# Kernel optimization log

Measured on AMD Instinct MI355X. Metric: run time of the kernel, lower is better.

## Reference

```python
import jax, jax.numpy as jnp
import numpy as np

NUM_PT = 13
NUM_SQ = 64
SQPT = NUM_SQ * NUM_PT            # 832
NUM_FEATURES = NUM_SQ * SQPT      # 53248
ATTN_TABLE = NUM_SQ * SQPT * SQPT # 44302336
DEPTH = 256
DFF = 1024
NUM_HEADS = 4
N = 512
LN_EPS = 1e-5


def layer_norm(x, w, b):
    m = jnp.mean(x, axis=-1, keepdims=True)
    v = jnp.mean(jnp.square(x - m), axis=-1, keepdims=True)
    return (x - m) * jax.lax.rsqrt(v + LN_EPS) * w + b


def setup_inputs() -> dict:
    key = jax.random.key(0)
    ks = jax.random.split(key, 12)
    # indices must satisfy piece_indices = ksq*832 + offset, offset in [0,832)
    pno = jax.random.randint(ks[0], (N, NUM_SQ), 0, SQPT, dtype=jnp.int32)
    ksq = jax.random.randint(ks[1], (N,), 0, NUM_SQ, dtype=jnp.int32)
    piece_indices = ksq[:, None] * SQPT + pno
    attn_bias_indices = jax.random.randint(ks[2], (N, NUM_SQ * NUM_SQ), 0, NUM_PT * NUM_PT, dtype=jnp.int32)
    f32 = jnp.float32
    return {
        "piece_indices": piece_indices,
        "attn_bias_indices": attn_bias_indices,
        "ksq": ksq,
        "value_table": jax.random.normal(ks[3], (NUM_FEATURES, DEPTH), f32) * 0.02,
        "attn_weights_table": jax.random.normal(ks[4], (ATTN_TABLE, NUM_HEADS), f32) * 0.02,
        "attn_bias_table": jax.random.normal(ks[5], (NUM_PT * NUM_PT, NUM_HEADS), f32) * 0.02,
        "attn_scale": jnp.asarray(100.0, f32),
        "W1": jax.random.normal(ks[6], (DEPTH, DFF), f32) * 0.02,
        "b1": jnp.zeros((DFF,), f32),
        "W2": jax.random.normal(ks[7], (DFF, DEPTH), f32) * 0.02,
        "b2": jnp.zeros((DEPTH,), f32),
        "ln1_w": jnp.ones((DEPTH,), f32),
        "ln1_b": jnp.zeros((DEPTH,), f32),
        "ln2_w": jnp.ones((DEPTH,), f32),
        "ln2_b": jnp.zeros((DEPTH,), f32),
    }


def reference(piece_indices, attn_bias_indices, ksq, value_table, attn_weights_table,
              attn_bias_table, attn_scale, W1, b1, W2, b2, ln1_w, ln1_b, ln2_w, ln2_b):
    n = piece_indices.shape[0]
    dh = DEPTH // NUM_HEADS
    pno = piece_indices - ksq[:, None] * SQPT                      # [N,64] in [0,832)
    attn_idx = (pno[:, :, None] * SQPT + pno[:, None, :]
                + ksq[:, None, None] * SQPT * SQPT)                # [N,64,64]
    aw = attn_weights_table[attn_idx]                              # [N,64,64,H]
    abi = attn_bias_indices.reshape(n, NUM_SQ, NUM_SQ).transpose(0, 2, 1)
    ab = attn_bias_table[abi]                                      # [N,64,64,H]
    logits = ((aw + ab) * attn_scale).transpose(0, 3, 1, 2)        # [N,H,64,64]
    attn = jax.nn.softmax(logits, axis=-1)
    values = value_table[piece_indices].reshape(n, NUM_SQ, NUM_HEADS, dh).transpose(0, 2, 1, 3)  # [N,H,64,dh]
    ctx = jnp.einsum('nhqk,nhkd->nhqd', attn, values) + values
    x = layer_norm(ctx.transpose(0, 2, 1, 3).reshape(n, NUM_SQ, DEPTH), ln1_w, ln1_b)
    ffn = jnp.maximum(x @ W1 + b1, 0.0) @ W2 + b2
    return layer_norm(ffn + x, ln2_w, ln2_b)
```

## Files before the change

### kernel.cpp

```cpp
#include <hip/hip_runtime.h>
#include <stdint.h>

typedef unsigned short u16;
typedef __attribute__((ext_vector_type(8))) short bf16x8;
typedef __attribute__((ext_vector_type(4))) float f32x4;

typedef __attribute__((address_space(1))) const unsigned char gas_u8;
typedef __attribute__((address_space(3))) unsigned char las_u8;

__device__ __forceinline__ void gload_lds16(const void* g, void* l) {
  __builtin_amdgcn_global_load_lds((const gas_u8*)g, (las_u8*)l, 16, 0, 0);
}

__device__ __forceinline__ u16 f2bf(float f) {
  uint32_t u = __float_as_uint(f);
  u += 0x7fffu + ((u >> 16) & 1u);
  return (u16)(u >> 16);
}
__device__ __forceinline__ float bf2f(u16 v) {
  return __uint_as_float(((uint32_t)v) << 16);
}

__global__ __launch_bounds__(256, 4)
void transpose_kernel(const float* __restrict__ W1, u16* __restrict__ W1T,
                      const float* __restrict__ W2, u16* __restrict__ W2T) {
  __shared__ u16 tile[64 * 66];
  int b = blockIdx.x;
  const float* src; u16* dst; int R, C, tc, tr;
  if (b < 64) { src = W1; dst = W1T; R = 256; C = 1024; tc = (b & 15) * 64; tr = (b >> 4) * 64; }
  else { b -= 64; src = W2; dst = W2T; R = 1024; C = 256; tc = (b & 3) * 64; tr = (b >> 2) * 64; }
  const int t = threadIdx.x;
  const int c = t & 63, rb = t >> 6;
#pragma unroll
  for (int i = 0; i < 16; ++i) {
    int r = i * 4 + rb;
    tile[r * 66 + c] = f2bf(src[(size_t)(tr + r) * C + tc + c]);
  }
  __syncthreads();
#pragma unroll
  for (int i = 0; i < 16; ++i) {
    int x = i * 4 + rb;
    int y = c;
    dst[(size_t)(tc + x) * R + tr + y] = tile[y * 66 + x];
  }
}

__global__ __launch_bounds__(256, 2)
void attn_kernel(const int* __restrict__ piece_indices,
                 const int* __restrict__ abi_idx,
                 const int* __restrict__ ksq,
                 const float* __restrict__ value_table,
                 const float* __restrict__ aw_table,
                 const float* __restrict__ ab_table,
                 const float* __restrict__ scale_p,
                 const float* __restrict__ ln1w, const float* __restrict__ ln1b,
                 u16* __restrict__ xout) {
  __shared__ __align__(16) u16 VT[256 * 64];
  __shared__ __align__(16) u16 P[4 * 64 * 64];
  __shared__ __align__(16) float abt_s[169 * 4];
  __shared__ int pno_s[64];
  __shared__ int pidx_s[64];
  __shared__ float red[4][64][2];
  __shared__ float redA[4][4][64];
  __shared__ float redB[4][4][64];

  const int n = blockIdx.x;
  const int t = threadIdx.x;
  const int h = t >> 6;
  const int lane = t & 63;
  const int ks = ksq[n];

  if (t < 64) {
    int pi = piece_indices[n * 64 + t];
    pidx_s[t] = pi;
    pno_s[t] = pi - ks * 832;
  }
  for (int i = t; i < 676; i += 256) abt_s[i] = ab_table[i];
  __syncthreads();

  const float scale = scale_p[0];
  const int q = lane, kg = h;

  float l[4][16];
  {
    const int base = ks * (832 * 832) + pno_s[q] * 832;
#pragma unroll
    for (int j = 0; j < 16; ++j) {
      int k = kg * 16 + j;
      int idx = base + pno_s[k];
      f32x4 aw4 = *(const f32x4*)(aw_table + (size_t)idx * 4);
      int bi = abi_idx[n * 4096 + k * 64 + q];
      f32x4 ab4 = *(const f32x4*)(abt_s + bi * 4);
#pragma unroll
      for (int hh = 0; hh < 4; ++hh) l[hh][j] = (aw4[hh] + ab4[hh]) * scale;
    }
  }

  {
    const int feat = t;
#pragma unroll
    for (int c = 0; c < 8; ++c) {
      bf16x8 vv;
#pragma unroll
      for (int j = 0; j < 8; ++j) {
        int k = c * 8 + j;
        float v = value_table[(size_t)pidx_s[k] * 256 + feat];
        vv[j] = (short)f2bf(v);
      }
      int off = feat * 64 + ((c ^ (feat & 7)) << 3);
      *(bf16x8*)(&VT[off]) = vv;
    }
  }

#pragma unroll
  for (int hh = 0; hh < 4; ++hh) {
    float m = l[hh][0];
#pragma unroll
    for (int j = 1; j < 16; ++j) m = fmaxf(m, l[hh][j]);
    redA[kg][hh][q] = m;
  }
  __syncthreads();
  float gmax[4], inv[4];
#pragma unroll
  for (int hh = 0; hh < 4; ++hh) {
    float m = fmaxf(fmaxf(redA[0][hh][q], redA[1][hh][q]),
                    fmaxf(redA[2][hh][q], redA[3][hh][q]));
    gmax[hh] = m;
    float s = 0.f;
#pragma unroll
    for (int j = 0; j < 16; ++j) { l[hh][j] = __expf(l[hh][j] - m); s += l[hh][j]; }
    redB[kg][hh][q] = s;
  }
  __syncthreads();
#pragma unroll
  for (int hh = 0; hh < 4; ++hh)
    inv[hh] = 1.f / (redB[0][hh][q] + redB[1][hh][q] + redB[2][hh][q] + redB[3][hh][q]);

#pragma unroll
  for (int hh = 0; hh < 4; ++hh) {
#pragma unroll
    for (int c2 = 0; c2 < 2; ++c2) {
      int c = kg * 2 + c2;
      bf16x8 pv;
#pragma unroll
      for (int j8 = 0; j8 < 8; ++j8) {
        int j = c2 * 8 + j8;
        int k = kg * 16 + j;
        float v = l[hh][j] * inv[hh] + ((k == q) ? 1.f : 0.f);
        pv[j8] = (short)f2bf(v);
      }
      int off = (hh * 64 + q) * 64 + ((c ^ (q & 7)) << 3);
      *(bf16x8*)(&P[off]) = pv;
    }
  }
  __syncthreads();

  const int li = lane & 15, lg = lane >> 4;
  f32x4 acc[4][4] = {};
#pragma unroll
  for (int kst = 0; kst < 2; ++kst) {
    int cg = kst * 4 + lg;
    bf16x8 aF[4], bF[4];
#pragma unroll
    for (int mi = 0; mi < 4; ++mi) {
      int row = mi * 16 + li;
      aF[mi] = *(const bf16x8*)(&P[(h * 64 + row) * 64 + ((cg ^ (row & 7)) << 3)]);
    }
#pragma unroll
    for (int ni = 0; ni < 4; ++ni) {
      int rr = h * 64 + ni * 16 + li;
      bF[ni] = *(const bf16x8*)(&VT[rr * 64 + ((cg ^ (rr & 7)) << 3)]);
    }
#pragma unroll
    for (int mi = 0; mi < 4; ++mi)
#pragma unroll
      for (int ni = 0; ni < 4; ++ni)
        acc[mi][ni] = __builtin_amdgcn_mfma_f32_16x16x32_bf16(aF[mi], bF[ni], acc[mi][ni], 0, 0, 0);
  }

#pragma unroll
  for (int mi = 0; mi < 4; ++mi)
#pragma unroll
    for (int r = 0; r < 4; ++r) {
      float s1 = 0.f, s2 = 0.f;
#pragma unroll
      for (int ni = 0; ni < 4; ++ni) { float v = acc[mi][ni][r]; s1 += v; s2 += v * v; }
#pragma unroll
      for (int mk = 1; mk < 16; mk <<= 1) { s1 += __shfl_xor(s1, mk, 64); s2 += __shfl_xor(s2, mk, 64); }
      if (li == 0) { int q2 = mi * 16 + lg * 4 + r; red[h][q2][0] = s1; red[h][q2][1] = s2; }
    }
  __syncthreads();

  float w_[4], b_[4];
#pragma unroll
  for (int ni = 0; ni < 4; ++ni) {
    int f = h * 64 + ni * 16 + li;
    w_[ni] = ln1w[f]; b_[ni] = ln1b[f];
  }
#pragma unroll
  for (int mi = 0; mi < 4; ++mi)
#pragma unroll
    for (int r = 0; r < 4; ++r) {
      int q2 = mi * 16 + lg * 4 + r;
      float S1 = red[0][q2][0] + red[1][q2][0] + red[2][q2][0] + red[3][q2][0];
      float S2 = red[0][q2][1] + red[1][q2][1] + red[2][q2][1] + red[3][q2][1];
      float mean = S1 * (1.f / 256.f);
      float var = S2 * (1.f / 256.f) - mean * mean;
      float rs = rsqrtf(var + 1e-5f);
      size_t tb = (size_t)(n * 64 + q2) * 256;
#pragma unroll
      for (int ni = 0; ni < 4; ++ni) {
        float xv = (acc[mi][ni][r] - mean) * rs * w_[ni] + b_[ni];
        xout[tb + h * 64 + ni * 16 + li] = f2bf(xv);
      }
    }
}

__global__ __launch_bounds__(256, 2)
void ffn1_kernel(const u16* __restrict__ X, const u16* __restrict__ W1T,
                 const float* __restrict__ b1, u16* __restrict__ H) {
  __shared__ __align__(16) u16 A_lds[64 * 64];
  __shared__ __align__(16) u16 B_lds[256 * 64];
  const int t = threadIdx.x;
  const int wv = t >> 6, lane = t & 63;
  const int li = lane & 15, lg = lane >> 4;
  const int m0 = blockIdx.x * 64;
  const int bn0 = blockIdx.y * 256;
  f32x4 acc[4][4] = {};

  for (int k0 = 0; k0 < 256; k0 += 64) {
    if (k0) __syncthreads();
#pragma unroll
    for (int it = 0; it < 2; ++it) {
      int idx = it * 256 + t;
      int row = idx >> 3, c = idx & 7;
      const u16* g = X + (size_t)(m0 + row) * 256 + k0 + ((c ^ (row & 7)) << 3);
      gload_lds16(g, (char*)A_lds + it * 4096 + wv * 1024);
    }
#pragma unroll
    for (int it = 0; it < 8; ++it) {
      int idx = it * 256 + t;
      int row = idx >> 3, c = idx & 7;
      const u16* g = W1T + (size_t)(bn0 + row) * 256 + k0 + ((c ^ (row & 7)) << 3);
      gload_lds16(g, (char*)B_lds + it * 4096 + wv * 1024);
    }
    __syncthreads();
#pragma unroll
    for (int kst = 0; kst < 2; ++kst) {
      int cg = kst * 4 + lg;
      bf16x8 aF[4], bF[4];
#pragma unroll
      for (int mi = 0; mi < 4; ++mi) {
        int row = mi * 16 + li;
        aF[mi] = *(const bf16x8*)(&A_lds[row * 64 + ((cg ^ (row & 7)) << 3)]);
      }
#pragma unroll
      for (int ni = 0; ni < 4; ++ni) {
        int row = wv * 64 + ni * 16 + li;
        bF[ni] = *(const bf16x8*)(&B_lds[row * 64 + ((cg ^ (row & 7)) << 3)]);
      }
#pragma unroll
      for (int mi = 0; mi < 4; ++mi)
#pragma unroll
        for (int ni = 0; ni < 4; ++ni)
          acc[mi][ni] = __builtin_amdgcn_mfma_f32_16x16x32_bf16(aF[mi], bF[ni], acc[mi][ni], 0, 0, 0);
    }
  }

  float bias[4];
#pragma unroll
  for (int ni = 0; ni < 4; ++ni) bias[ni] = b1[bn0 + wv * 64 + ni * 16 + li];
#pragma unroll
  for (int mi = 0; mi < 4; ++mi)
#pragma unroll
    for (int r = 0; r < 4; ++r) {
      int row = m0 + mi * 16 + lg * 4 + r;
#pragma unroll
      for (int ni = 0; ni < 4; ++ni) {
        float v = fmaxf(acc[mi][ni][r] + bias[ni], 0.f);
        H[(size_t)row * 1024 + bn0 + wv * 64 + ni * 16 + li] = f2bf(v);
      }
    }
}

__global__ __launch_bounds__(256, 2)
void ffn2_kernel(const u16* __restrict__ Hm, const u16* __restrict__ W2T,
                 const float* __restrict__ b2, const u16* __restrict__ X,
                 const float* __restrict__ ln2w, const float* __restrict__ ln2b,
                 float* __restrict__ out) {
  __shared__ __align__(16) u16 A_lds[64 * 64];
  __shared__ __align__(16) u16 B_lds[256 * 64];
  __shared__ float red[4][64][2];
  const int t = threadIdx.x;
  const int wv = t >> 6, lane = t & 63;
  const int li = lane & 15, lg = lane >> 4;
  const int m0 = blockIdx.x * 64;
  f32x4 acc[4][4] = {};

  for (int k0 = 0; k0 < 1024; k0 += 64) {
    if (k0) __syncthreads();
#pragma unroll
    for (int it = 0; it < 2; ++it) {
      int idx = it * 256 + t;
      int row = idx >> 3, c = idx & 7;
      const u16* g = Hm + (size_t)(m0 + row) * 1024 + k0 + ((c ^ (row & 7)) << 3);
      gload_lds16(g, (char*)A_lds + it * 4096 + wv * 1024);
    }
#pragma unroll
    for (int it = 0; it < 8; ++it) {
      int idx = it * 256 + t;
      int row = idx >> 3, c = idx & 7;
      const u16* g = W2T + (size_t)row * 1024 + k0 + ((c ^ (row & 7)) << 3);
      gload_lds16(g, (char*)B_lds + it * 4096 + wv * 1024);
    }
    __syncthreads();
#pragma unroll
    for (int kst = 0; kst < 2; ++kst) {
      int cg = kst * 4 + lg;
      bf16x8 aF[4], bF[4];
#pragma unroll
      for (int mi = 0; mi < 4; ++mi) {
        int row = mi * 16 + li;
        aF[mi] = *(const bf16x8*)(&A_lds[row * 64 + ((cg ^ (row & 7)) << 3)]);
      }
#pragma unroll
      for (int ni = 0; ni < 4; ++ni) {
        int row = wv * 64 + ni * 16 + li;
        bF[ni] = *(const bf16x8*)(&B_lds[row * 64 + ((cg ^ (row & 7)) << 3)]);
      }
#pragma unroll
      for (int mi = 0; mi < 4; ++mi)
#pragma unroll
        for (int ni = 0; ni < 4; ++ni)
          acc[mi][ni] = __builtin_amdgcn_mfma_f32_16x16x32_bf16(aF[mi], bF[ni], acc[mi][ni], 0, 0, 0);
    }
  }
  __syncthreads();

  float bias2[4];
#pragma unroll
  for (int ni = 0; ni < 4; ++ni) bias2[ni] = b2[wv * 64 + ni * 16 + li];

#pragma unroll
  for (int mi = 0; mi < 4; ++mi)
#pragma unroll
    for (int r = 0; r < 4; ++r) {
      float s1 = 0.f, s2 = 0.f;
      int row = m0 + mi * 16 + lg * 4 + r;
#pragma unroll
      for (int ni = 0; ni < 4; ++ni) {
        int col = wv * 64 + ni * 16 + li;
        float v = acc[mi][ni][r] + bias2[ni] + bf2f(X[(size_t)row * 256 + col]);
        acc[mi][ni][r] = v;
        s1 += v; s2 += v * v;
      }
#pragma unroll
      for (int mk = 1; mk < 16; mk <<= 1) { s1 += __shfl_xor(s1, mk, 64); s2 += __shfl_xor(s2, mk, 64); }
      if (li == 0) { int q2 = mi * 16 + lg * 4 + r; red[wv][q2][0] = s1; red[wv][q2][1] = s2; }
    }
  __syncthreads();

  float lw[4], lb[4];
#pragma unroll
  for (int ni = 0; ni < 4; ++ni) {
    int col = wv * 64 + ni * 16 + li;
    lw[ni] = ln2w[col]; lb[ni] = ln2b[col];
  }
#pragma unroll
  for (int mi = 0; mi < 4; ++mi)
#pragma unroll
    for (int r = 0; r < 4; ++r) {
      int q2 = mi * 16 + lg * 4 + r;
      float S1 = red[0][q2][0] + red[1][q2][0] + red[2][q2][0] + red[3][q2][0];
      float S2 = red[0][q2][1] + red[1][q2][1] + red[2][q2][1] + red[3][q2][1];
      float mean = S1 * (1.f / 256.f);
      float var = S2 * (1.f / 256.f) - mean * mean;
      float rs = rsqrtf(var + 1e-5f);
      size_t rbase = (size_t)(m0 + q2) * 256;
#pragma unroll
      for (int ni = 0; ni < 4; ++ni)
        out[rbase + wv * 64 + ni * 16 + li] = (acc[mi][ni][r] - mean) * rs * lw[ni] + lb[ni];
    }
}

extern "C" void kernel_launch(void* const* d_in, const int* in_sizes, int n_in,
                              void* d_out, int out_size, void* d_ws, size_t ws_size,
                              hipStream_t stream) {
  const int* piece_indices = (const int*)d_in[0];
  const int* abi_idx       = (const int*)d_in[1];
  const int* ksq           = (const int*)d_in[2];
  const float* value_table = (const float*)d_in[3];
  const float* aw_table    = (const float*)d_in[4];
  const float* ab_table    = (const float*)d_in[5];
  const float* attn_scale  = (const float*)d_in[6];
  const float* W1          = (const float*)d_in[7];
  const float* b1          = (const float*)d_in[8];
  const float* W2          = (const float*)d_in[9];
  const float* b2          = (const float*)d_in[10];
  const float* ln1w        = (const float*)d_in[11];
  const float* ln1b        = (const float*)d_in[12];
  const float* ln2w        = (const float*)d_in[13];
  const float* ln2b        = (const float*)d_in[14];

  char* ws = (char*)d_ws;
  u16* W1T = (u16*)(ws);
  u16* W2T = (u16*)(ws + (512 << 10));
  u16* X   = (u16*)(ws + (1 << 20));
  u16* Hm  = (u16*)(ws + (1 << 20) + (16 << 20));
  float* out = (float*)d_out;

  transpose_kernel<<<128, 256, 0, stream>>>(W1, W1T, W2, W2T);
  attn_kernel<<<512, 256, 0, stream>>>(piece_indices, abi_idx, ksq, value_table,
                                       aw_table, ab_table, attn_scale, ln1w, ln1b, X);
  ffn1_kernel<<<dim3(512, 4), 256, 0, stream>>>(X, W1T, b1, Hm);
  ffn2_kernel<<<512, 256, 0, stream>>>(Hm, W2T, b2, X, ln2w, ln2b, out);
}
```

Before: 127.5 us.

## Fuse FFN1 and FFN2 into one kernel keeping hidden activations in LDS

Merges the two FFN GEMM kernels into one. Each 64-row block keeps its X tile resident in LDS and walks the 1024-wide hidden dimension in chunks of 64, computing ReLU(X·W1+b1) for each chunk into LDS and immediately accumulating it into the second GEMM. This removes the 16MB global write and reread of the hidden activations and one kernel launch, and the residual is read from LDS. In exchange, grid parallelism drops from 2048 to 512 blocks, there is no load/compute overlap, and LDS use per block is larger, which may limit occupancy.

```diff
diff --git a/kernel.cpp b/kernel.cpp
--- a/kernel.cpp
+++ b/kernel.cpp
@@ -120,12 +120,11 @@
     redA[kg][hh][q] = m;
   }
   __syncthreads();
-  float gmax[4], inv[4];
+  float inv[4];
 #pragma unroll
   for (int hh = 0; hh < 4; ++hh) {
     float m = fmaxf(fmaxf(redA[0][hh][q], redA[1][hh][q]),
                     fmaxf(redA[2][hh][q], redA[3][hh][q]));
-    gmax[hh] = m;
     float s = 0.f;
 #pragma unroll
     for (int j = 0; j < 16; ++j) { l[hh][j] = __expf(l[hh][j] - m); s += l[hh][j]; }
@@ -217,34 +216,82 @@
 }
 
 __global__ __launch_bounds__(256, 2)
-void ffn1_kernel(const u16* __restrict__ X, const u16* __restrict__ W1T,
-                 const float* __restrict__ b1, u16* __restrict__ H) {
-  __shared__ __align__(16) u16 A_lds[64 * 64];
-  __shared__ __align__(16) u16 B_lds[256 * 64];
+void ffn_fused_kernel(const u16* __restrict__ X, const u16* __restrict__ W1T,
+                      const u16* __restrict__ W2T,
+                      const float* __restrict__ b1, const float* __restrict__ b2,
+                      const float* __restrict__ ln2w, const float* __restrict__ ln2b,
+                      float* __restrict__ out) {
+  __shared__ __align__(16) u16 Xl[64 * 256];
+  __shared__ __align__(16) u16 Wb[64 * 256];
+  __shared__ __align__(16) u16 Hb[64 * 64];
+  __shared__ float red[4][64][2];
+
   const int t = threadIdx.x;
   const int wv = t >> 6, lane = t & 63;
   const int li = lane & 15, lg = lane >> 4;
   const int m0 = blockIdx.x * 64;
-  const int bn0 = blockIdx.y * 256;
-  f32x4 acc[4][4] = {};
-
-  for (int k0 = 0; k0 < 256; k0 += 64) {
-    if (k0) __syncthreads();
-#pragma unroll
-    for (int it = 0; it < 2; ++it) {
+  f32x4 oacc[4][4] = {};
+
+#pragma unroll
+  for (int it = 0; it < 8; ++it) {
+    int idx = it * 256 + t;
+    int row = idx >> 5, c = idx & 31;
+    const u16* g = X + (size_t)(m0 + row) * 256 + (((c ^ (row & 7)) & 31) << 3);
+    gload_lds16(g, (char*)Xl + it * 4096 + wv * 1024);
+  }
+
+  for (int ch = 0; ch < 16; ++ch) {
+#pragma unroll
+    for (int it = 0; it < 8; ++it) {
       int idx = it * 256 + t;
-      int row = idx >> 3, c = idx & 7;
-      const u16* g = X + (size_t)(m0 + row) * 256 + k0 + ((c ^ (row & 7)) << 3);
-      gload_lds16(g, (char*)A_lds + it * 4096 + wv * 1024);
+      int row = idx >> 5, c = idx & 31;
+      const u16* g = W1T + (size_t)(ch * 64 + row) * 256 + (((c ^ (row & 7)) & 31) << 3);
+      gload_lds16(g, (char*)Wb + it * 4096 + wv * 1024);
+    }
+    __syncthreads();
+
+    f32x4 hacc[4] = {};
+#pragma unroll
+    for (int kst = 0; kst < 8; ++kst) {
+      int cg = kst * 4 + lg;
+      bf16x8 aF[4], bF;
+      {
+        int brow = wv * 16 + li;
+        bF = *(const bf16x8*)((char*)Wb + brow * 512 + (((cg ^ (brow & 7)) & 31) << 4));
+      }
+#pragma unroll
+      for (int mi = 0; mi < 4; ++mi) {
+        int row = mi * 16 + li;
+        aF[mi] = *(const bf16x8*)((char*)Xl + row * 512 + (((cg ^ (row & 7)) & 31) << 4));
+      }
+#pragma unroll
+      for (int mi = 0; mi < 4; ++mi)
+        hacc[mi] = __builtin_amdgcn_mfma_f32_16x16x32_bf16(aF[mi], bF, hacc[mi], 0, 0, 0);
+    }
+    __syncthreads();
+
+    {
+      float bv = b1[ch * 64 + wv * 16 + li];
+      int col = wv * 16 + li;
+      int c2 = col >> 3;
+#pragma unroll
+      for (int mi = 0; mi < 4; ++mi)
+#pragma unroll
+        for (int r = 0; r < 4; ++r) {
+          int row = mi * 16 + lg * 4 + r;
+          float v = fmaxf(hacc[mi][r] + bv, 0.f);
+          *(u16*)((char*)Hb + row * 128 + ((c2 ^ (row & 7)) << 4) + (col & 7) * 2) = f2bf(v);
+        }
     }
 #pragma unroll
     for (int it = 0; it < 8; ++it) {
       int idx = it * 256 + t;
       int row = idx >> 3, c = idx & 7;
-      const u16* g = W1T + (size_t)(bn0 + row) * 256 + k0 + ((c ^ (row & 7)) << 3);
-      gload_lds16(g, (char*)B_lds + it * 4096 + wv * 1024);
+      const u16* g = W2T + (size_t)row * 1024 + ch * 64 + ((c ^ (row & 7)) << 3);
+      gload_lds16(g, (char*)Wb + it * 4096 + wv * 1024);
     }
     __syncthreads();
+
 #pragma unroll
     for (int kst = 0; kst < 2; ++kst) {
       int cg = kst * 4 + lg;
@@ -252,90 +299,21 @@
 #pragma unroll
       for (int mi = 0; mi < 4; ++mi) {
         int row = mi * 16 + li;
-        aF[mi] = *(const bf16x8*)(&A_lds[row * 64 + ((cg ^ (row & 7)) << 3)]);
+        aF[mi] = *(const bf16x8*)((char*)Hb + row * 128 + (((cg ^ (row & 7)) & 7) << 4));
       }
 #pragma unroll
       for (int ni = 0; ni < 4; ++ni) {
         int row = wv * 64 + ni * 16 + li;
-        bF[ni] = *(const bf16x8*)(&B_lds[row * 64 + ((cg ^ (row & 7)) << 3)]);
+        bF[ni] = *(const bf16x8*)((char*)Wb + row * 128 + (((cg ^ (row & 7)) & 7) << 4));
       }
 #pragma unroll
       for (int mi = 0; mi < 4; ++mi)
 #pragma unroll
         for (int ni = 0; ni < 4; ++ni)
-          acc[mi][ni] = __builtin_amdgcn_mfma_f32_16x16x32_bf16(aF[mi], bF[ni], acc[mi][ni], 0, 0, 0);
-    }
-  }
-
-  float bias[4];
-#pragma unroll
-  for (int ni = 0; ni < 4; ++ni) bias[ni] = b1[bn0 + wv * 64 + ni * 16 + li];
-#pragma unroll
-  for (int mi = 0; mi < 4; ++mi)
-#pragma unroll
-    for (int r = 0; r < 4; ++r) {
-      int row = m0 + mi * 16 + lg * 4 + r;
-#pragma unroll
-      for (int ni = 0; ni < 4; ++ni) {
-        float v = fmaxf(acc[mi][ni][r] + bias[ni], 0.f);
-        H[(size_t)row * 1024 + bn0 + wv * 64 + ni * 16 + li] = f2bf(v);
-      }
-    }
-}
-
-__global__ __launch_bounds__(256, 2)
-void ffn2_kernel(const u16* __restrict__ Hm, const u16* __restrict__ W2T,
-                 const float* __restrict__ b2, const u16* __restrict__ X,
-                 const float* __restrict__ ln2w, const float* __restrict__ ln2b,
-                 float* __restrict__ out) {
-  __shared__ __align__(16) u16 A_lds[64 * 64];
-  __shared__ __align__(16) u16 B_lds[256 * 64];
-  __shared__ float red[4][64][2];
-  const int t = threadIdx.x;
-  const int wv = t >> 6, lane = t & 63;
-  const int li = lane & 15, lg = lane >> 4;
-  const int m0 = blockIdx.x * 64;
-  f32x4 acc[4][4] = {};
-
-  for (int k0 = 0; k0 < 1024; k0 += 64) {
-    if (k0) __syncthreads();
-#pragma unroll
-    for (int it = 0; it < 2; ++it) {
-      int idx = it * 256 + t;
-      int row = idx >> 3, c = idx & 7;
-      const u16* g = Hm + (size_t)(m0 + row) * 1024 + k0 + ((c ^ (row & 7)) << 3);
-      gload_lds16(g, (char*)A_lds + it * 4096 + wv * 1024);
-    }
-#pragma unroll
-    for (int it = 0; it < 8; ++it) {
-      int idx = it * 256 + t;
-      int row = idx >> 3, c = idx & 7;
-      const u16* g = W2T + (size_t)row * 1024 + k0 + ((c ^ (row & 7)) << 3);
-      gload_lds16(g, (char*)B_lds + it * 4096 + wv * 1024);
+          oacc[mi][ni] = __builtin_amdgcn_mfma_f32_16x16x32_bf16(aF[mi], bF[ni], oacc[mi][ni], 0, 0, 0);
     }
     __syncthreads();
-#pragma unroll
-    for (int kst = 0; kst < 2; ++kst) {
-      int cg = kst * 4 + lg;
-      bf16x8 aF[4], bF[4];
-#pragma unroll
-      for (int mi = 0; mi < 4; ++mi) {
-        int row = mi * 16 + li;
-        aF[mi] = *(const bf16x8*)(&A_lds[row * 64 + ((cg ^ (row & 7)) << 3)]);
-      }
-#pragma unroll
-      for (int ni = 0; ni < 4; ++ni) {
-        int row = wv * 64 + ni * 16 + li;
-        bF[ni] = *(const bf16x8*)(&B_lds[row * 64 + ((cg ^ (row & 7)) << 3)]);
-      }
-#pragma unroll
-      for (int mi = 0; mi < 4; ++mi)
-#pragma unroll
-        for (int ni = 0; ni < 4; ++ni)
-          acc[mi][ni] = __builtin_amdgcn_mfma_f32_16x16x32_bf16(aF[mi], bF[ni], acc[mi][ni], 0, 0, 0);
-    }
-  }
-  __syncthreads();
+  }
 
   float bias2[4];
 #pragma unroll
@@ -346,12 +324,14 @@
 #pragma unroll
     for (int r = 0; r < 4; ++r) {
       float s1 = 0.f, s2 = 0.f;
-      int row = m0 + mi * 16 + lg * 4 + r;
+      int row = mi * 16 + lg * 4 + r;
 #pragma unroll
       for (int ni = 0; ni < 4; ++ni) {
         int col = wv * 64 + ni * 16 + li;
-        float v = acc[mi][ni][r] + bias2[ni] + bf2f(X[(size_t)row * 256 + col]);
-        acc[mi][ni][r] = v;
+        int cc = col >> 3;
+        u16 xres = *(const u16*)((char*)Xl + row * 512 + (((cc ^ (row & 7)) & 31) << 4) + (col & 7) * 2);
+        float v = oacc[mi][ni][r] + bias2[ni] + bf2f(xres);
+        oacc[mi][ni][r] = v;
         s1 += v; s2 += v * v;
       }
 #pragma unroll
@@ -379,7 +359,7 @@
       size_t rbase = (size_t)(m0 + q2) * 256;
 #pragma unroll
       for (int ni = 0; ni < 4; ++ni)
-        out[rbase + wv * 64 + ni * 16 + li] = (acc[mi][ni][r] - mean) * rs * lw[ni] + lb[ni];
+        out[rbase + wv * 64 + ni * 16 + li] = (oacc[mi][ni][r] - mean) * rs * lw[ni] + lb[ni];
     }
 }
 
@@ -406,12 +386,10 @@
   u16* W1T = (u16*)(ws);
   u16* W2T = (u16*)(ws + (512 << 10));
   u16* X   = (u16*)(ws + (1 << 20));
-  u16* Hm  = (u16*)(ws + (1 << 20) + (16 << 20));
   float* out = (float*)d_out;
 
   transpose_kernel<<<128, 256, 0, stream>>>(W1, W1T, W2, W2T);
   attn_kernel<<<512, 256, 0, stream>>>(piece_indices, abi_idx, ksq, value_table,
                                        aw_table, ab_table, attn_scale, ln1w, ln1b, X);
-  ffn1_kernel<<<dim3(512, 4), 256, 0, stream>>>(X, W1T, b1, Hm);
-  ffn2_kernel<<<512, 256, 0, stream>>>(Hm, W2T, b2, X, ln2w, ln2b, out);
-}
+  ffn_fused_kernel<<<512, 256, 0, stream>>>(X, W1T, W2T, b1, b2, ln2w, ln2b, out);
+}
```

Measured after the change: 119.0 us. 1.07x faster.
